# Performance work log

Hardware: AMD Instinct MI355X
Metric: run time of the kernel (lower is better)

## Reference

```python
import jax, jax.numpy as jnp
import numpy as np

B, S, IN1, IN2, H = 1024, 200, 128, 128, 128

def setup_inputs() -> dict:
    key = jax.random.key(0)
    k = jax.random.split(key, 8)
    inp = jax.random.normal(k[0], (B, S, IN1), dtype=jnp.float32)
    z = jax.random.normal(k[1], (B, IN2), dtype=jnp.float32)
    mask = jax.random.randint(k[2], (B, S), 0, 2, dtype=jnp.int32)
    # learned params (PyTorch Linear: y = x @ W.T + b; store transposed for x @ W)
    W1 = jax.random.normal(k[3], (IN1, H), dtype=jnp.float32) / np.sqrt(IN1)
    W2 = jax.random.normal(k[4], (IN2, H), dtype=jnp.float32) / np.sqrt(IN2)
    b2 = jax.random.normal(k[5], (H,), dtype=jnp.float32) * 0.02
    V = jax.random.normal(k[6], (H, 1), dtype=jnp.float32) / np.sqrt(H)
    bV = jax.random.normal(k[7], (1,), dtype=jnp.float32) * 0.02
    return {"input": inp, "z": z, "mask": mask, "W1": W1, "W2": W2, "b2": b2, "V": V, "bV": bV}

def reference(input, z, mask, W1, W2, b2, V, bV):
    # w1h: [B,S,H]; w2h: [B,1,H]
    w1h = jnp.einsum('bsd,dh->bsh', input, W1)
    w2h = (z @ W2 + b2)[:, None, :]
    u = jnp.tanh(w1h + w2h)                      # [B,S,H]
    att = (jnp.einsum('bsh,h->bs', u, V[:, 0]) + bV[0])  # [B,S]
    att = jnp.where(mask == 0, jnp.float32(-1e10), att)
    att = jax.nn.softmax(att, axis=1)            # softmax over S
    out = jnp.einsum('bs,bsd->bd', att, input)   # weighted sum pooling
    return out
```

## Files before the change

### kernel.cpp

```cpp
#include <hip/hip_runtime.h>
#include <hip/hip_bf16.h>

constexpr int S_ = 200;
constexpr int SP = 208;

typedef __attribute__((ext_vector_type(8))) short short8_t;
typedef __attribute__((ext_vector_type(4))) float float4_t;

__device__ inline unsigned short f2bf(float f) {
  unsigned int u = __float_as_uint(f);
  u += 0x7FFFu + ((u >> 16) & 1u);
  return (unsigned short)(u >> 16);
}
__device__ inline float bf2f(unsigned int us) {
  return __uint_as_float(us << 16);
}

__global__ __launch_bounds__(256, 2) void m2o_attn_kernel(
    const float* __restrict__ input, const float* __restrict__ z,
    const int* __restrict__ mask, const float* __restrict__ W1,
    const float* __restrict__ W2, const float* __restrict__ b2,
    const float* __restrict__ V, const float* __restrict__ bV,
    float* __restrict__ out) {
  __shared__ __align__(16) unsigned short in_lds[SP * 128];
  __shared__ float att_part[4][SP];
  __shared__ float w2h_lds[128];
  __shared__ float att_w[SP];
  __shared__ float pool[4][128];
  __shared__ float redA[4], redB[4];

  const int t = threadIdx.x;
  const int b = blockIdx.x;
  const int lane = t & 63;
  const int wid = t >> 6;

  const float4* inp4 = reinterpret_cast<const float4*>(input + (size_t)b * (S_ * 128));
  #pragma unroll
  for (int i = 0; i < 25; ++i) {
    int f = t + i * 256;
    float4 v = inp4[f];
    int s = f >> 5;
    int d0 = (f & 31) << 2;
    int idx = s * 128 + (d0 ^ ((s & 7) << 3));
    unsigned int lo = (unsigned int)f2bf(v.x) | ((unsigned int)f2bf(v.y) << 16);
    unsigned int hi = (unsigned int)f2bf(v.z) | ((unsigned int)f2bf(v.w) << 16);
    *reinterpret_cast<uint2*>(&in_lds[idx]) = make_uint2(lo, hi);
  }
  {
    unsigned int* p32 = reinterpret_cast<unsigned int*>(in_lds);
    for (int i = t; i < 8 * 64; i += 256) p32[200 * 64 + i] = 0u;
  }
  if (t < 128) {
    float acc = b2[t];
    const float* zb = z + (size_t)b * 128;
    for (int d = 0; d < 128; ++d) acc += zb[d] * W2[d * 128 + t];
    w2h_lds[t] = acc;
  }
  const int hb = wid * 32;
  short8_t bfrag[2][4];
  #pragma unroll
  for (int n = 0; n < 2; ++n) {
    int h = hb + n * 16 + (lane & 15);
    #pragma unroll
    for (int kk = 0; kk < 4; ++kk) {
      short8_t fr;
      #pragma unroll
      for (int j = 0; j < 8; ++j) {
        int k = (lane >> 4) * 8 + j + kk * 32;
        fr[j] = (short)f2bf(W1[k * 128 + h]);
      }
      bfrag[n][kk] = fr;
    }
  }
  const float v0 = V[hb + (lane & 15)];
  const float v1 = V[hb + 16 + (lane & 15)];

  __syncthreads();

  const float w0 = w2h_lds[hb + (lane & 15)];
  const float w1v = w2h_lds[hb + 16 + (lane & 15)];

  for (int mt = 0; mt < 13; ++mt) {
    float4_t acc0 = {0.f, 0.f, 0.f, 0.f};
    float4_t acc1 = {0.f, 0.f, 0.f, 0.f};
    const int arow = mt * 16 + (lane & 15);
    const int swz = (arow & 7) << 3;
    #pragma unroll
    for (int kk = 0; kk < 4; ++kk) {
      const int k0 = (lane >> 4) * 8 + kk * 32;
      const short8_t a = *reinterpret_cast<const short8_t*>(
          &in_lds[arow * 128 + (k0 ^ swz)]);
      acc0 = __builtin_amdgcn_mfma_f32_16x16x32_bf16(a, bfrag[0][kk], acc0, 0, 0, 0);
      acc1 = __builtin_amdgcn_mfma_f32_16x16x32_bf16(a, bfrag[1][kk], acc1, 0, 0, 0);
    }
    #pragma unroll
    for (int r = 0; r < 4; ++r) {
      float x0 = fminf(10.f, fmaxf(-10.f, acc0[r] + w0));
      float x1 = fminf(10.f, fmaxf(-10.f, acc1[r] + w1v));
      float t0 = __expf(2.f * x0);
      float t1 = __expf(2.f * x1);
      float u0 = 1.f - __fdividef(2.f, t0 + 1.f);
      float u1 = 1.f - __fdividef(2.f, t1 + 1.f);
      float p = u0 * v0 + u1 * v1;
      p += __shfl_xor(p, 1);
      p += __shfl_xor(p, 2);
      p += __shfl_xor(p, 4);
      p += __shfl_xor(p, 8);
      if ((lane & 15) == 0)
        att_part[wid][mt * 16 + (lane >> 4) * 4 + r] = p;
    }
  }
  __syncthreads();

  float logit = -3.0e38f, e = 0.f;
  {
    float val;
    if (t < S_) {
      val = att_part[0][t] + att_part[1][t] + att_part[2][t] + att_part[3][t] + bV[0];
      if (mask[(size_t)b * S_ + t] == 0) val = -1e10f;
    } else {
      val = -3.0e38f;
    }
    logit = val;
    float m = val;
    #pragma unroll
    for (int off = 32; off; off >>= 1) m = fmaxf(m, __shfl_xor(m, off));
    if (lane == 0) redA[wid] = m;
  }
  __syncthreads();
  {
    float M = fmaxf(fmaxf(redA[0], redA[1]), fmaxf(redA[2], redA[3]));
    e = (t < S_) ? __expf(logit - M) : 0.f;
    float sg = e;
    #pragma unroll
    for (int off = 32; off; off >>= 1) sg += __shfl_xor(sg, off);
    if (lane == 0) redB[wid] = sg;
  }
  __syncthreads();
  {
    float Ssum = redB[0] + redB[1] + redB[2] + redB[3];
    if (t < SP) att_w[t] = (t < S_) ? e / Ssum : 0.f;
  }
  __syncthreads();

  {
    const unsigned int* l32 = reinterpret_cast<const unsigned int*>(in_lds);
    const int p = t & 63;
    const int c = t >> 6;
    float a0 = 0.f, a1 = 0.f;
    for (int s = c * 50; s < c * 50 + 50; ++s) {
      float w = att_w[s];
      unsigned int u = l32[s * 64 + (p ^ ((s & 7) << 2))];
      a0 += w * bf2f(u & 0xffffu);
      a1 += w * bf2f(u >> 16);
    }
    pool[c][2 * p] = a0;
    pool[c][2 * p + 1] = a1;
  }
  __syncthreads();
  if (t < 128)
    out[(size_t)b * 128 + t] = pool[0][t] + pool[1][t] + pool[2][t] + pool[3][t];
}

extern "C" void kernel_launch(void* const* d_in, const int* in_sizes, int n_in,
                              void* d_out, int out_size, void* d_ws, size_t ws_size,
                              hipStream_t stream) {
  const float* input = (const float*)d_in[0];
  const float* z     = (const float*)d_in[1];
  const int*   mask  = (const int*)d_in[2];
  const float* W1    = (const float*)d_in[3];
  const float* W2    = (const float*)d_in[4];
  const float* b2    = (const float*)d_in[5];
  const float* V     = (const float*)d_in[6];
  const float* bV    = (const float*)d_in[7];
  float* out = (float*)d_out;
  m2o_attn_kernel<<<1024, 256, 0, stream>>>(input, z, mask, W1, W2, b2, V, bV, out);
}
```

Measured before the change: 206.7 us.

## Stream input tiles from global into registers instead of staging bf16 copy in LDS

Drops the large LDS staging buffer (about 52KB of bf16 input per block) and instead has each wave load its A-fragments directly from global memory as fp32, converting to bf16 in registers and prefetching the next tile while the current one runs. Work is split differently: waves cover 64 hidden columns and half the sequence, the z·W2 product is split across all threads, and the final pooling re-reads fp32 input from global/L2. The smaller LDS footprint allows raising launch bounds to 4 blocks per SM, trading extra global re-reads and register pressure for more occupancy. Pooling now uses full-precision input instead of the bf16 copy, and the tanh clamp is removed.

Result: faster. 196.2 us (-5.0%).

```diff
diff --git a/kernel.cpp b/kernel.cpp
--- a/kernel.cpp
+++ b/kernel.cpp
@@ -12,154 +12,176 @@
   u += 0x7FFFu + ((u >> 16) & 1u);
   return (unsigned short)(u >> 16);
 }
-__device__ inline float bf2f(unsigned int us) {
-  return __uint_as_float(us << 16);
-}
-
-__global__ __launch_bounds__(256, 2) void m2o_attn_kernel(
+__device__ inline unsigned int pk2(float x, float y) {
+  return (unsigned int)f2bf(x) | ((unsigned int)f2bf(y) << 16);
+}
+
+__global__ __launch_bounds__(256, 4) void m2o_attn_kernel(
     const float* __restrict__ input, const float* __restrict__ z,
     const int* __restrict__ mask, const float* __restrict__ W1,
     const float* __restrict__ W2, const float* __restrict__ b2,
     const float* __restrict__ V, const float* __restrict__ bV,
     float* __restrict__ out) {
-  __shared__ __align__(16) unsigned short in_lds[SP * 128];
-  __shared__ float att_part[4][SP];
-  __shared__ float w2h_lds[128];
+  __shared__ float w2h_part[2][128];
+  __shared__ float att_part[2][SP];
   __shared__ float att_w[SP];
-  __shared__ float pool[4][128];
+  __shared__ float pool[2][128];
   __shared__ float redA[4], redB[4];
 
   const int t = threadIdx.x;
   const int b = blockIdx.x;
   const int lane = t & 63;
   const int wid = t >> 6;
-
-  const float4* inp4 = reinterpret_cast<const float4*>(input + (size_t)b * (S_ * 128));
+  const int c = lane & 15;
+  const int kb = lane >> 4;
+
+  const float* inb = input + (size_t)b * (S_ * 128);
+
+  const int maskv = (t < S_) ? mask[(size_t)b * S_ + t] : 0;
+  const float bVv = bV[0];
+
+  {
+    const int h = t & 127, ph = t >> 7;
+    const float* zb = z + (size_t)b * 128 + ph * 64;
+    float acc = (ph == 0) ? b2[h] : 0.f;
+    #pragma unroll 8
+    for (int d = 0; d < 64; ++d) acc = fmaf(zb[d], W2[(ph * 64 + d) * 128 + h], acc);
+    w2h_part[ph][h] = acc;
+  }
+
+  const int hh = (wid & 1) * 64;
+  short8_t bfrag[4][4];
   #pragma unroll
-  for (int i = 0; i < 25; ++i) {
-    int f = t + i * 256;
-    float4 v = inp4[f];
-    int s = f >> 5;
-    int d0 = (f & 31) << 2;
-    int idx = s * 128 + (d0 ^ ((s & 7) << 3));
-    unsigned int lo = (unsigned int)f2bf(v.x) | ((unsigned int)f2bf(v.y) << 16);
-    unsigned int hi = (unsigned int)f2bf(v.z) | ((unsigned int)f2bf(v.w) << 16);
-    *reinterpret_cast<uint2*>(&in_lds[idx]) = make_uint2(lo, hi);
-  }
-  {
-    unsigned int* p32 = reinterpret_cast<unsigned int*>(in_lds);
-    for (int i = t; i < 8 * 64; i += 256) p32[200 * 64 + i] = 0u;
-  }
-  if (t < 128) {
-    float acc = b2[t];
-    const float* zb = z + (size_t)b * 128;
-    for (int d = 0; d < 128; ++d) acc += zb[d] * W2[d * 128 + t];
-    w2h_lds[t] = acc;
-  }
-  const int hb = wid * 32;
-  short8_t bfrag[2][4];
+  for (int n = 0; n < 4; ++n) {
+    const int h = hh + n * 16 + c;
+    #pragma unroll
+    for (int kk = 0; kk < 4; ++kk) {
+      union { short8_t s8; unsigned int u[4]; } cv;
+      #pragma unroll
+      for (int jp = 0; jp < 4; ++jp) {
+        const int k = kk * 32 + kb * 8 + jp * 2;
+        cv.u[jp] = pk2(W1[k * 128 + h], W1[(k + 1) * 128 + h]);
+      }
+      bfrag[n][kk] = cv.s8;
+    }
+  }
+  float vv[4];
   #pragma unroll
-  for (int n = 0; n < 2; ++n) {
-    int h = hb + n * 16 + (lane & 15);
-    #pragma unroll
-    for (int kk = 0; kk < 4; ++kk) {
-      short8_t fr;
-      #pragma unroll
-      for (int j = 0; j < 8; ++j) {
-        int k = (lane >> 4) * 8 + j + kk * 32;
-        fr[j] = (short)f2bf(W1[k * 128 + h]);
+  for (int n = 0; n < 4; ++n) vv[n] = V[hh + n * 16 + c];
+
+  __syncthreads();
+
+  float w2v[4];
+  #pragma unroll
+  for (int n = 0; n < 4; ++n) {
+    const int h = hh + n * 16 + c;
+    w2v[n] = w2h_part[0][h] + w2h_part[1][h];
+  }
+
+  const int half = wid >> 1;
+  const int pslot = wid & 1;
+  const int mt0 = half * 7;
+  const int nmt = half ? 6 : 7;
+
+  float4 pa[4][2];
+  {
+    const int arow = mt0 * 16 + c;
+    const int lrow = arow < S_ ? arow : (S_ - 1);
+    const float* rp = inb + lrow * 128 + kb * 8;
+    #pragma unroll
+    for (int kk = 0; kk < 4; ++kk) {
+      pa[kk][0] = *reinterpret_cast<const float4*>(rp + kk * 32);
+      pa[kk][1] = *reinterpret_cast<const float4*>(rp + kk * 32 + 4);
+    }
+  }
+
+  for (int i = 0; i < nmt; ++i) {
+    const int mt = mt0 + i;
+    short8_t a[4];
+    #pragma unroll
+    for (int kk = 0; kk < 4; ++kk) {
+      union { short8_t s8; unsigned int u[4]; } cv;
+      cv.u[0] = pk2(pa[kk][0].x, pa[kk][0].y);
+      cv.u[1] = pk2(pa[kk][0].z, pa[kk][0].w);
+      cv.u[2] = pk2(pa[kk][1].x, pa[kk][1].y);
+      cv.u[3] = pk2(pa[kk][1].z, pa[kk][1].w);
+      a[kk] = cv.s8;
+    }
+    if (i + 1 < nmt) {
+      const int arow = (mt + 1) * 16 + c;
+      const int lrow = arow < S_ ? arow : (S_ - 1);
+      const float* rp = inb + lrow * 128 + kb * 8;
+      #pragma unroll
+      for (int kk = 0; kk < 4; ++kk) {
+        pa[kk][0] = *reinterpret_cast<const float4*>(rp + kk * 32);
+        pa[kk][1] = *reinterpret_cast<const float4*>(rp + kk * 32 + 4);
       }
-      bfrag[n][kk] = fr;
-    }
-  }
-  const float v0 = V[hb + (lane & 15)];
-  const float v1 = V[hb + 16 + (lane & 15)];
-
-  __syncthreads();
-
-  const float w0 = w2h_lds[hb + (lane & 15)];
-  const float w1v = w2h_lds[hb + 16 + (lane & 15)];
-
-  for (int mt = 0; mt < 13; ++mt) {
-    float4_t acc0 = {0.f, 0.f, 0.f, 0.f};
-    float4_t acc1 = {0.f, 0.f, 0.f, 0.f};
-    const int arow = mt * 16 + (lane & 15);
-    const int swz = (arow & 7) << 3;
-    #pragma unroll
-    for (int kk = 0; kk < 4; ++kk) {
-      const int k0 = (lane >> 4) * 8 + kk * 32;
-      const short8_t a = *reinterpret_cast<const short8_t*>(
-          &in_lds[arow * 128 + (k0 ^ swz)]);
-      acc0 = __builtin_amdgcn_mfma_f32_16x16x32_bf16(a, bfrag[0][kk], acc0, 0, 0, 0);
-      acc1 = __builtin_amdgcn_mfma_f32_16x16x32_bf16(a, bfrag[1][kk], acc1, 0, 0, 0);
+    }
+    float4_t acc[4] = {{0.f, 0.f, 0.f, 0.f}, {0.f, 0.f, 0.f, 0.f},
+                       {0.f, 0.f, 0.f, 0.f}, {0.f, 0.f, 0.f, 0.f}};
+    #pragma unroll
+    for (int kk = 0; kk < 4; ++kk) {
+      #pragma unroll
+      for (int n = 0; n < 4; ++n)
+        acc[n] = __builtin_amdgcn_mfma_f32_16x16x32_bf16(a[kk], bfrag[n][kk], acc[n], 0, 0, 0);
     }
     #pragma unroll
     for (int r = 0; r < 4; ++r) {
-      float x0 = fminf(10.f, fmaxf(-10.f, acc0[r] + w0));
-      float x1 = fminf(10.f, fmaxf(-10.f, acc1[r] + w1v));
-      float t0 = __expf(2.f * x0);
-      float t1 = __expf(2.f * x1);
-      float u0 = 1.f - __fdividef(2.f, t0 + 1.f);
-      float u1 = 1.f - __fdividef(2.f, t1 + 1.f);
-      float p = u0 * v0 + u1 * v1;
+      const int row = mt * 16 + kb * 4 + r;
+      float p = 0.f;
+      #pragma unroll
+      for (int n = 0; n < 4; ++n) {
+        const float x = acc[n][r] + w2v[n];
+        const float e = __expf(x + x);
+        const float u = 1.f - __fdividef(2.f, e + 1.f);
+        p = fmaf(u, vv[n], p);
+      }
       p += __shfl_xor(p, 1);
       p += __shfl_xor(p, 2);
       p += __shfl_xor(p, 4);
       p += __shfl_xor(p, 8);
-      if ((lane & 15) == 0)
-        att_part[wid][mt * 16 + (lane >> 4) * 4 + r] = p;
-    }
-  }
-  __syncthreads();
-
-  float logit = -3.0e38f, e = 0.f;
-  {
-    float val;
-    if (t < S_) {
-      val = att_part[0][t] + att_part[1][t] + att_part[2][t] + att_part[3][t] + bV[0];
-      if (mask[(size_t)b * S_ + t] == 0) val = -1e10f;
-    } else {
-      val = -3.0e38f;
-    }
-    logit = val;
-    float m = val;
+      if (c == 0 && row < S_) att_part[pslot][row] = p;
+    }
+  }
+  __syncthreads();
+
+  float logit = -3.0e38f, ee = 0.f;
+  if (t < S_) {
+    logit = att_part[0][t] + att_part[1][t] + bVv;
+    if (maskv == 0) logit = -1e10f;
+  }
+  {
+    float m = logit;
     #pragma unroll
     for (int off = 32; off; off >>= 1) m = fmaxf(m, __shfl_xor(m, off));
     if (lane == 0) redA[wid] = m;
   }
   __syncthreads();
   {
-    float M = fmaxf(fmaxf(redA[0], redA[1]), fmaxf(redA[2], redA[3]));
-    e = (t < S_) ? __expf(logit - M) : 0.f;
-    float sg = e;
+    const float M = fmaxf(fmaxf(redA[0], redA[1]), fmaxf(redA[2], redA[3]));
+    ee = (t < S_) ? __expf(logit - M) : 0.f;
+    float sg = ee;
     #pragma unroll
     for (int off = 32; off; off >>= 1) sg += __shfl_xor(sg, off);
     if (lane == 0) redB[wid] = sg;
   }
   __syncthreads();
   {
-    float Ssum = redB[0] + redB[1] + redB[2] + redB[3];
-    if (t < SP) att_w[t] = (t < S_) ? e / Ssum : 0.f;
-  }
-  __syncthreads();
-
-  {
-    const unsigned int* l32 = reinterpret_cast<const unsigned int*>(in_lds);
-    const int p = t & 63;
-    const int c = t >> 6;
-    float a0 = 0.f, a1 = 0.f;
-    for (int s = c * 50; s < c * 50 + 50; ++s) {
-      float w = att_w[s];
-      unsigned int u = l32[s * 64 + (p ^ ((s & 7) << 2))];
-      a0 += w * bf2f(u & 0xffffu);
-      a1 += w * bf2f(u >> 16);
-    }
-    pool[c][2 * p] = a0;
-    pool[c][2 * p + 1] = a1;
-  }
-  __syncthreads();
-  if (t < 128)
-    out[(size_t)b * 128 + t] = pool[0][t] + pool[1][t] + pool[2][t] + pool[3][t];
+    const float Ssum = redB[0] + redB[1] + redB[2] + redB[3];
+    if (t < SP) att_w[t] = (t < S_) ? __fdividef(ee, Ssum) : 0.f;
+  }
+  __syncthreads();
+
+  {
+    const int d = t & 127, ph = t >> 7;
+    const float* pp = inb + (size_t)(ph * 100) * 128 + d;
+    float a0 = 0.f;
+    #pragma unroll 4
+    for (int s = 0; s < 100; ++s) a0 = fmaf(att_w[ph * 100 + s], pp[s * 128], a0);
+    pool[ph][d] = a0;
+  }
+  __syncthreads();
+  if (t < 128) out[(size_t)b * 128 + t] = pool[0][t] + pool[1][t];
 }
 
 extern "C" void kernel_launch(void* const* d_in, const int* in_sizes, int n_in,
```
